# Optimization experiments

Hardware: AMD Instinct MI355X
Metric: run time of the kernel (lower is better)

## Reference

```python
import jax, jax.numpy as jnp
import numpy as np

NUM_HEADS = 8


def _conv1x1(x, W, b):
    # 1x1 conv == per-pixel linear: x [N,C,H,W], W [O,C], b [O]
    return jnp.einsum('nchw,oc->nohw', x, W) + b[None, :, None, None]


def setup_inputs() -> dict:
    key = jax.random.key(0)
    ks = jax.random.split(key, 10)
    C = 512
    s = 1.0 / np.sqrt(C)  # keep pre-softmax logits in a sane range
    return {
        'x': jax.random.normal(ks[0], (2, C, 64, 64), dtype=jnp.float32),
        'Wq': jax.random.normal(ks[1], (C, C), dtype=jnp.float32) * s,
        'bq': jax.random.normal(ks[2], (C,), dtype=jnp.float32) * 0.01,
        'Wk': jax.random.normal(ks[3], (C, C), dtype=jnp.float32) * s,
        'bk': jax.random.normal(ks[4], (C,), dtype=jnp.float32) * 0.01,
        'Wv': jax.random.normal(ks[5], (C, C), dtype=jnp.float32) * s,
        'bv': jax.random.normal(ks[6], (C,), dtype=jnp.float32) * 0.01,
        'Wo': jax.random.normal(ks[7], (C, C), dtype=jnp.float32) * s,
        'bo': jax.random.normal(ks[8], (C,), dtype=jnp.float32) * 0.01,
        'gamma': jax.random.normal(ks[9], (1,), dtype=jnp.float32),
    }


def reference(x, Wq, bq, Wk, bk, Wv, bv, Wo, bo, gamma):
    N, C, H, W = x.shape
    nh = NUM_HEADS
    hd = C // nh
    S = H * W
    scale = 1.0 / (hd ** 0.5)
    # Projections via 1x1 conv, then split heads over flattened spatial tokens
    Q = _conv1x1(x, Wq, bq).reshape(N, nh, hd, S).transpose(0, 1, 3, 2)  # [N,h,S,d]
    K = _conv1x1(x, Wk, bk).reshape(N, nh, hd, S)                         # [N,h,d,S]
    V = _conv1x1(x, Wv, bv).reshape(N, nh, hd, S).transpose(0, 1, 3, 2)  # [N,h,S,d]
    attn = jax.nn.softmax(jnp.einsum('nhsd,nhdt->nhst', Q, K) * scale, axis=-1)
    out = jnp.einsum('nhst,nhtd->nhsd', attn, V)                          # [N,h,S,d]
    out = out.transpose(0, 1, 3, 2).reshape(N, C, H, W)
    out = _conv1x1(out, Wo, bo)
    return gamma[0] * out + x
```

## Files before the change

kernel.cpp:

```cpp
#include <hip/hip_runtime.h>
#include <hip/hip_bf16.h>

typedef __attribute__((ext_vector_type(4))) float f32x4;
typedef __attribute__((ext_vector_type(16))) float f32x16;
typedef __attribute__((ext_vector_type(8))) short s16x8;
typedef __attribute__((ext_vector_type(4))) unsigned short us16x4;
typedef __attribute__((ext_vector_type(4))) unsigned int u32x4;

#define C_DIM 512
#define S_DIM 4096
#define NB 2
#define NH 8
#define HD 64

#define QSCALE 0.1803368801111244f

__device__ __forceinline__ unsigned short f2bf(float f) {
    union { float f; unsigned u; } v; v.f = f;
    unsigned r = v.u + 0x7FFFu + ((v.u >> 16) & 1u);
    return (unsigned short)(r >> 16);
}

__device__ __forceinline__ float bf2f(unsigned short u) {
    union { unsigned u; float f; } v; v.u = ((unsigned)u) << 16;
    return v.f;
}

__device__ __forceinline__ float dev_exp2(float x) {
    float r;
    asm("v_exp_f32 %0, %1" : "=v"(r) : "v"(x));
    return r;
}

__device__ __forceinline__ unsigned cvt_pk_bf16(float lo, float hi) {
    unsigned r;
    asm("v_cvt_pk_bf16_f32 %0, %1, %2" : "=v"(r) : "v"(lo), "v"(hi));
    return r;
}

__device__ __forceinline__ void lane_swap(unsigned& a, unsigned& b) {
    asm("v_permlane32_swap_b32 %0, %1" : "+v"(a), "+v"(b));
}

__device__ __forceinline__ void gload_lds16(const void* g, void* l) {
    __builtin_amdgcn_global_load_lds(
        (const __attribute__((address_space(1))) void*)g,
        (__attribute__((address_space(3))) void*)l, 16, 0, 0);
}

__global__ __launch_bounds__(256) void wconv_kernel(
    const float* __restrict__ Wq, const float* __restrict__ Wk,
    const float* __restrict__ Wv, const float* __restrict__ Wo,
    unsigned short* __restrict__ Wb) {
    int i = blockIdx.x * 256 + threadIdx.x;
    int y = blockIdx.y;
    const float* src = (y == 0) ? Wq : (y == 1) ? Wk : (y == 2) ? Wv : Wo;
    Wb[(size_t)y * 262144 + i] = f2bf(src[i]);
}

__global__ __launch_bounds__(256) void xpose_kernel(
    const float* __restrict__ x, unsigned short* __restrict__ Xt) {
    __shared__ float tile[32][33];
    int n = blockIdx.z;
    int s0 = blockIdx.x * 32;
    int c0 = blockIdx.y * 32;
    int tx = threadIdx.x & 31;
    int ty = threadIdx.x >> 5;
#pragma unroll
    for (int r = 0; r < 4; ++r) {
        int c = c0 + ty + r * 8;
        tile[ty + r * 8][tx] = x[((size_t)n * C_DIM + c) * S_DIM + s0 + tx];
    }
    __syncthreads();
#pragma unroll
    for (int r = 0; r < 4; ++r) {
        int s = s0 + ty + r * 8;
        Xt[((size_t)n * S_DIM + s) * C_DIM + c0 + tx] = f2bf(tile[tx][ty + r * 8]);
    }
}

__global__ __launch_bounds__(256) void qkv_gemm_kernel(
    const unsigned short* __restrict__ Wb, const unsigned short* __restrict__ Xt,
    const float* __restrict__ bq, const float* __restrict__ bk, const float* __restrict__ bv,
    unsigned short* __restrict__ Qt, unsigned short* __restrict__ Kt,
    unsigned short* __restrict__ Vb) {
    __shared__ unsigned short As[128 * 64];
    __shared__ unsigned short Bs[128 * 64];
    int w = blockIdx.z >> 1;
    int n = blockIdx.z & 1;
    const unsigned short* A = Wb + (size_t)w * 262144;
    const unsigned short* B = Xt + (size_t)n * S_DIM * C_DIM;
    int tid = threadIdx.x;
    int wid = tid >> 6, lane = tid & 63;
    int wm = wid >> 1, wn = wid & 1;
    int lr = lane & 15, lq = lane >> 4;
    int bm = blockIdx.y * 128, bt = blockIdx.x * 128;
    int r_in = lane >> 3, c8 = (lane & 7) * 8;

    f32x4 zero = {0.f, 0.f, 0.f, 0.f};
    f32x4 acc[4][4];
#pragma unroll
    for (int i = 0; i < 4; ++i)
#pragma unroll
        for (int j = 0; j < 4; ++j) acc[i][j] = zero;

    for (int ks = 0; ks < 8; ++ks) {
#pragma unroll
        for (int q = 0; q < 4; ++q) {
            int row = wid * 32 + q * 8;
            gload_lds16(A + (size_t)(bm + row + r_in) * C_DIM + ks * 64 + c8, &As[row * 64]);
            gload_lds16(B + (size_t)(bt + row + r_in) * C_DIM + ks * 64 + c8, &Bs[row * 64]);
        }
        __syncthreads();
#pragma unroll
        for (int kk = 0; kk < 2; ++kk) {
            s16x8 af[4], bf[4];
#pragma unroll
            for (int i = 0; i < 4; ++i)
                af[i] = *(const s16x8*)&As[(wm * 64 + i * 16 + lr) * 64 + kk * 32 + lq * 8];
#pragma unroll
            for (int j = 0; j < 4; ++j)
                bf[j] = *(const s16x8*)&Bs[(wn * 64 + j * 16 + lr) * 64 + kk * 32 + lq * 8];
#pragma unroll
            for (int i = 0; i < 4; ++i)
#pragma unroll
                for (int j = 0; j < 4; ++j)
                    acc[i][j] = __builtin_amdgcn_mfma_f32_16x16x32_bf16(af[i], bf[j], acc[i][j], 0, 0, 0);
        }
        __syncthreads();
    }

    const float* bias = (w == 0) ? bq : (w == 1) ? bk : bv;
#pragma unroll
    for (int i = 0; i < 4; ++i) {
        int obase = bm + wm * 64 + i * 16 + lq * 4;
#pragma unroll
        for (int j = 0; j < 4; ++j) {
            int t = bt + wn * 64 + j * 16 + lr;
            if (w == 0) {
                us16x4 pk;
#pragma unroll
                for (int r = 0; r < 4; ++r)
                    pk[r] = f2bf((acc[i][j][r] + bias[obase + r]) * QSCALE);
                int h = obase >> 6, d = obase & 63;
                *(us16x4*)&Qt[(((size_t)(n * NH + h) * S_DIM) + t) * HD + d] = pk;
            } else if (w == 1) {
                us16x4 pk;
#pragma unroll
                for (int r = 0; r < 4; ++r) pk[r] = f2bf(acc[i][j][r] + bias[obase + r]);
                int h = obase >> 6, d = obase & 63;
                *(us16x4*)&Kt[(((size_t)(n * NH + h) * S_DIM) + t) * HD + d] = pk;
            } else {
#pragma unroll
                for (int r = 0; r < 4; ++r) {
                    int o = obase + r;
                    Vb[((size_t)(n * C_DIM + o)) * S_DIM + t] = f2bf(acc[i][j][r] + bias[o]);
                }
            }
        }
    }
}

__global__ __launch_bounds__(256) void attn_kernel(
    const unsigned short* __restrict__ Qt, const unsigned short* __restrict__ Kt,
    const unsigned short* __restrict__ Vb, unsigned short* __restrict__ Opart,
    float* __restrict__ Lpart) {
    __shared__ unsigned short Ks[2][64 * 64];
    __shared__ unsigned short Vs[2][64 * 64];
    int tid = threadIdx.x, wid = tid >> 6, lane = tid & 63;
    int l31 = lane & 31, hi = lane >> 5;
    int radj = (l31 & 7) ^ ((l31 >> 3) & 3);

    int bidl = blockIdx.x;
    int swz = (bidl & 7) * 128 + (bidl >> 3);
    int nh = swz >> 6;
    int rem = swz & 63;
    int qb = rem >> 1;
    int half = rem & 1;
    int n = nh >> 3, h = nh & 7;
    int qrow0 = qb * 128 + wid * 32;
    int kvbase = half * 2048;

    const unsigned short* Qh = Qt + (size_t)nh * S_DIM * HD;
    const unsigned short* Kh = Kt + (size_t)nh * S_DIM * HD;
    const unsigned short* Vh = Vb + ((size_t)(n * C_DIM + h * HD)) * S_DIM;

    s16x8 qf[4];
#pragma unroll
    for (int st = 0; st < 4; ++st)
        qf[st] = *(const s16x8*)&Qh[((size_t)(qrow0 + l31)) * HD + st * 16 + hi * 8];

    s16x8 ones;
#pragma unroll
    for (int r = 0; r < 8; ++r) ones[r] = (short)0x3F80;

    f32x16 Oacc[2], Lacc;
#pragma unroll
    for (int jm = 0; jm < 2; ++jm)
#pragma unroll
        for (int r = 0; r < 16; ++r) Oacc[jm][r] = 0.f;
#pragma unroll
    for (int r = 0; r < 16; ++r) Lacc[r] = 0.f;

    int srow0 = tid >> 3, sslot = tid & 7;
    int wslot = (sslot ^ (srow0 & 7) ^ ((srow0 >> 3) & 3)) * 8;

    s16x8 kreg[2], vreg[2];
#pragma unroll
    for (int q = 0; q < 2; ++q) {
        int row = srow0 + q * 32;
        kreg[q] = *(const s16x8*)&Kh[((size_t)(kvbase + row)) * HD + sslot * 8];
        vreg[q] = *(const s16x8*)&Vh[((size_t)row) * S_DIM + kvbase + sslot * 8];
    }
#pragma unroll
    for (int q = 0; q < 2; ++q) {
        int row = srow0 + q * 32;
        *(s16x8*)&Ks[0][row * 64 + wslot] = kreg[q];
        *(s16x8*)&Vs[0][row * 64 + wslot] = vreg[q];
    }
    __syncthreads();

    for (int kt = 0; kt < 32; ++kt) {
        int cur = kt & 1;
        if (kt < 31) {
#pragma unroll
            for (int q = 0; q < 2; ++q) {
                int row = srow0 + q * 32;
                kreg[q] = *(const s16x8*)&Kh[((size_t)(kvbase + (kt + 1) * 64 + row)) * HD + sslot * 8];
                vreg[q] = *(const s16x8*)&Vh[((size_t)row) * S_DIM + kvbase + (kt + 1) * 64 + sslot * 8];
            }
        }

        f32x16 s_[2];
#pragma unroll
        for (int jm = 0; jm < 2; ++jm) {
#pragma unroll
            for (int r = 0; r < 16; ++r) s_[jm][r] = 0.f;
            int arow = jm * 32 + l31;
#pragma unroll
            for (int st = 0; st < 4; ++st) {
                s16x8 kf = *(const s16x8*)&Ks[cur][arow * 64 + ((2 * st + hi) ^ radj) * 8];
                s_[jm] = __builtin_amdgcn_mfma_f32_32x32x16_bf16(kf, qf[st], s_[jm], 0, 0, 0);
            }
        }

        s16x8 pf[2][2];
#pragma unroll
        for (int jm = 0; jm < 2; ++jm) {
            unsigned pk0 = cvt_pk_bf16(dev_exp2(s_[jm][0]),  dev_exp2(s_[jm][1]));
            unsigned pk1 = cvt_pk_bf16(dev_exp2(s_[jm][2]),  dev_exp2(s_[jm][3]));
            unsigned pk2 = cvt_pk_bf16(dev_exp2(s_[jm][4]),  dev_exp2(s_[jm][5]));
            unsigned pk3 = cvt_pk_bf16(dev_exp2(s_[jm][6]),  dev_exp2(s_[jm][7]));
            unsigned pk4 = cvt_pk_bf16(dev_exp2(s_[jm][8]),  dev_exp2(s_[jm][9]));
            unsigned pk5 = cvt_pk_bf16(dev_exp2(s_[jm][10]), dev_exp2(s_[jm][11]));
            unsigned pk6 = cvt_pk_bf16(dev_exp2(s_[jm][12]), dev_exp2(s_[jm][13]));
            unsigned pk7 = cvt_pk_bf16(dev_exp2(s_[jm][14]), dev_exp2(s_[jm][15]));
            lane_swap(pk2, pk0);
            lane_swap(pk3, pk1);
            lane_swap(pk6, pk4);
            lane_swap(pk7, pk5);
            u32x4 w0 = {pk0, pk1, pk2, pk3};
            u32x4 w1 = {pk4, pk5, pk6, pk7};
            pf[jm][0] = __builtin_bit_cast(s16x8, w0);
            pf[jm][1] = __builtin_bit_cast(s16x8, w1);
        }

#pragma unroll
        for (int jm = 0; jm < 2; ++jm)
#pragma unroll
            for (int st = 0; st < 2; ++st)
                Lacc = __builtin_amdgcn_mfma_f32_32x32x16_bf16(ones, pf[jm][st], Lacc, 0, 0, 0);

#pragma unroll
        for (int jm2 = 0; jm2 < 2; ++jm2) {
            int vrow = jm2 * 32 + l31;
#pragma unroll
            for (int jm = 0; jm < 2; ++jm)
#pragma unroll
                for (int st = 0; st < 2; ++st) {
                    s16x8 vf = *(const s16x8*)&Vs[cur][vrow * 64 + ((jm * 4 + st * 2 + hi) ^ radj) * 8];
                    Oacc[jm2] = __builtin_amdgcn_mfma_f32_32x32x16_bf16(vf, pf[jm][st], Oacc[jm2], 0, 0, 0);
                }
        }

        if (kt < 31) {
            int nxt = cur ^ 1;
#pragma unroll
            for (int q = 0; q < 2; ++q) {
                int row = srow0 + q * 32;
                *(s16x8*)&Ks[nxt][row * 64 + wslot] = kreg[q];
                *(s16x8*)&Vs[nxt][row * 64 + wslot] = vreg[q];
            }
            __syncthreads();
        }
    }

    int token = qrow0 + l31;
    unsigned short* obase = Opart + (((size_t)(half * 16 + nh) * S_DIM + token) * HD);
#pragma unroll
    for (int jm2 = 0; jm2 < 2; ++jm2)
#pragma unroll
        for (int rq = 0; rq < 4; ++rq) {
            int d = jm2 * 32 + 8 * rq + 4 * hi;
            us16x4 pk;
#pragma unroll
            for (int r = 0; r < 4; ++r) pk[r] = f2bf(Oacc[jm2][rq * 4 + r]);
            *(us16x4*)&obase[d] = pk;
        }
    if (hi == 0)
        Lpart[(size_t)(half * 16 + nh) * S_DIM + token] = Lacc[0];
}

__global__ __launch_bounds__(256) void combine_kernel(
    const unsigned short* __restrict__ Opart, const float* __restrict__ Lpart,
    unsigned short* __restrict__ Ot) {
    int g = blockIdx.x * 256 + threadIdx.x;
    int d4 = (g & 15) * 4;
    int s = (g >> 4) & 4095;
    int nh = g >> 16;
    size_t base0 = ((size_t)nh * S_DIM + s) * HD + d4;
    size_t base1 = base0 + (size_t)16 * S_DIM * HD;
    us16x4 o0 = *(const us16x4*)&Opart[base0];
    us16x4 o1 = *(const us16x4*)&Opart[base1];
    float l = Lpart[(size_t)nh * S_DIM + s] + Lpart[(size_t)(16 + nh) * S_DIM + s];
    float inv = 1.f / l;
    int n = nh >> 3, h = nh & 7;
    us16x4 pk;
#pragma unroll
    for (int r = 0; r < 4; ++r) pk[r] = f2bf((bf2f(o0[r]) + bf2f(o1[r])) * inv);
    *(us16x4*)&Ot[((size_t)n * S_DIM + s) * C_DIM + h * HD + d4] = pk;
}

__global__ __launch_bounds__(256) void out_gemm_kernel(
    const unsigned short* __restrict__ Wb, const unsigned short* __restrict__ Ot,
    const float* __restrict__ bo, const float* __restrict__ gamma,
    const float* __restrict__ xin, float* __restrict__ out) {
    __shared__ unsigned short As[128 * 64];
    __shared__ unsigned short Bs[128 * 64];
    int n = blockIdx.z;
    const unsigned short* A = Wb + (size_t)3 * 262144;
    const unsigned short* B = Ot + (size_t)n * S_DIM * C_DIM;
    int tid = threadIdx.x;
    int wid = tid >> 6, lane = tid & 63;
    int wm = wid >> 1, wn = wid & 1;
    int lr = lane & 15, lq = lane >> 4;
    int bm = blockIdx.y * 128, bt = blockIdx.x * 128;
    int r_in = lane >> 3, c8 = (lane & 7) * 8;

    f32x4 zero = {0.f, 0.f, 0.f, 0.f};
    f32x4 acc[4][4];
#pragma unroll
    for (int i = 0; i < 4; ++i)
#pragma unroll
        for (int j = 0; j < 4; ++j) acc[i][j] = zero;

    for (int ks = 0; ks < 8; ++ks) {
#pragma unroll
        for (int q = 0; q < 4; ++q) {
            int row = wid * 32 + q * 8;
            gload_lds16(A + (size_t)(bm + row + r_in) * C_DIM + ks * 64 + c8, &As[row * 64]);
            gload_lds16(B + (size_t)(bt + row + r_in) * C_DIM + ks * 64 + c8, &Bs[row * 64]);
        }
        __syncthreads();
#pragma unroll
        for (int kk = 0; kk < 2; ++kk) {
            s16x8 af[4], bf[4];
#pragma unroll
            for (int i = 0; i < 4; ++i)
                af[i] = *(const s16x8*)&As[(wm * 64 + i * 16 + lr) * 64 + kk * 32 + lq * 8];
#pragma unroll
            for (int j = 0; j < 4; ++j)
                bf[j] = *(const s16x8*)&Bs[(wn * 64 + j * 16 + lr) * 64 + kk * 32 + lq * 8];
#pragma unroll
            for (int i = 0; i < 4; ++i)
#pragma unroll
                for (int j = 0; j < 4; ++j)
                    acc[i][j] = __builtin_amdgcn_mfma_f32_16x16x32_bf16(af[i], bf[j], acc[i][j], 0, 0, 0);
        }
        __syncthreads();
    }

    float g = gamma[0];
#pragma unroll
    for (int i = 0; i < 4; ++i) {
        int obase = bm + wm * 64 + i * 16 + lq * 4;
#pragma unroll
        for (int j = 0; j < 4; ++j) {
            int t = bt + wn * 64 + j * 16 + lr;
#pragma unroll
            for (int r = 0; r < 4; ++r) {
                int o = obase + r;
                size_t idx = ((size_t)(n * C_DIM + o)) * S_DIM + t;
                out[idx] = g * (acc[i][j][r] + bo[o]) + xin[idx];
            }
        }
    }
}

extern "C" void kernel_launch(void* const* d_in, const int* in_sizes, int n_in,
                              void* d_out, int out_size, void* d_ws, size_t ws_size,
                              hipStream_t stream) {
    const float* x  = (const float*)d_in[0];
    const float* Wq = (const float*)d_in[1];
    const float* bq = (const float*)d_in[2];
    const float* Wk = (const float*)d_in[3];
    const float* bk = (const float*)d_in[4];
    const float* Wv = (const float*)d_in[5];
    const float* bv = (const float*)d_in[6];
    const float* Wo = (const float*)d_in[7];
    const float* bo = (const float*)d_in[8];
    const float* gamma = (const float*)d_in[9];
    float* out = (float*)d_out;

    char* ws = (char*)d_ws;
    unsigned short* Wb = (unsigned short*)ws;
    unsigned short* Xt = (unsigned short*)(ws + ((size_t)2  << 20));
    unsigned short* Qt = (unsigned short*)(ws + ((size_t)10 << 20));
    unsigned short* Kt = (unsigned short*)(ws + ((size_t)18 << 20));
    unsigned short* Vb = (unsigned short*)(ws + ((size_t)26 << 20));
    unsigned short* Ot = (unsigned short*)(ws + ((size_t)34 << 20));
    unsigned short* Opart = (unsigned short*)(ws + ((size_t)42 << 20));
    float* Lpart = (float*)(ws + ((size_t)60 << 20));

    wconv_kernel<<<dim3(1024, 4), 256, 0, stream>>>(Wq, Wk, Wv, Wo, Wb);
    xpose_kernel<<<dim3(128, 16, 2), 256, 0, stream>>>(x, Xt);
    qkv_gemm_kernel<<<dim3(32, 4, 6), 256, 0, stream>>>(Wb, Xt, bq, bk, bv, Qt, Kt, Vb);
    attn_kernel<<<1024, 256, 0, stream>>>(Qt, Kt, Vb, Opart, Lpart);
    combine_kernel<<<4096, 256, 0, stream>>>(Opart, Lpart, Ot);
    out_gemm_kernel<<<dim3(32, 4, 2), 256, 0, stream>>>(Wb, Ot, bo, gamma, x, out);
}
```

Before: 157.5 us.

## Single-buffer K/V LDS tiles, raise MFMA wave priority, seed QK with zero accumulator

The attention kernel drops from double-buffered to single-buffered K/V tiles in shared memory, halving LDS use so more blocks can be resident per CU. Each iteration now stores the prefetched registers to LDS at the top, synchronises, and synchronises again at the end before the next overwrite. MFMA sections are wrapped in s_setprio so waves doing matrix math get issue priority over waves doing softmax or loads. The first QK MFMA takes a zero vector as accumulator instead of zeroing s_ in a separate loop. The cost is a second barrier per iteration and less overlap within a block, which is traded for occupancy.

```diff
diff --git a/kernel.cpp b/kernel.cpp
--- a/kernel.cpp
+++ b/kernel.cpp
@@ -165,8 +165,8 @@
     const unsigned short* __restrict__ Qt, const unsigned short* __restrict__ Kt,
     const unsigned short* __restrict__ Vb, unsigned short* __restrict__ Opart,
     float* __restrict__ Lpart) {
-    __shared__ unsigned short Ks[2][64 * 64];
-    __shared__ unsigned short Vs[2][64 * 64];
+    __shared__ unsigned short Ks[64 * 64];
+    __shared__ unsigned short Vs[64 * 64];
     int tid = threadIdx.x, wid = tid >> 6, lane = tid & 63;
     int l31 = lane & 31, hi = lane >> 5;
     int radj = (l31 & 7) ^ ((l31 >> 3) & 3);
@@ -193,6 +193,9 @@
     s16x8 ones;
 #pragma unroll
     for (int r = 0; r < 8; ++r) ones[r] = (short)0x3F80;
+    f32x16 fz;
+#pragma unroll
+    for (int r = 0; r < 16; ++r) fz[r] = 0.f;
 
     f32x16 Oacc[2], Lacc;
 #pragma unroll
@@ -212,16 +215,15 @@
         kreg[q] = *(const s16x8*)&Kh[((size_t)(kvbase + row)) * HD + sslot * 8];
         vreg[q] = *(const s16x8*)&Vh[((size_t)row) * S_DIM + kvbase + sslot * 8];
     }
-#pragma unroll
-    for (int q = 0; q < 2; ++q) {
-        int row = srow0 + q * 32;
-        *(s16x8*)&Ks[0][row * 64 + wslot] = kreg[q];
-        *(s16x8*)&Vs[0][row * 64 + wslot] = vreg[q];
-    }
-    __syncthreads();
 
     for (int kt = 0; kt < 32; ++kt) {
-        int cur = kt & 1;
+#pragma unroll
+        for (int q = 0; q < 2; ++q) {
+            int row = srow0 + q * 32;
+            *(s16x8*)&Ks[row * 64 + wslot] = kreg[q];
+            *(s16x8*)&Vs[row * 64 + wslot] = vreg[q];
+        }
+        __syncthreads();
         if (kt < 31) {
 #pragma unroll
             for (int q = 0; q < 2; ++q) {
@@ -232,17 +234,19 @@
         }
 
         f32x16 s_[2];
+        __builtin_amdgcn_s_setprio(1);
 #pragma unroll
         for (int jm = 0; jm < 2; ++jm) {
-#pragma unroll
-            for (int r = 0; r < 16; ++r) s_[jm][r] = 0.f;
             int arow = jm * 32 + l31;
-#pragma unroll
-            for (int st = 0; st < 4; ++st) {
-                s16x8 kf = *(const s16x8*)&Ks[cur][arow * 64 + ((2 * st + hi) ^ radj) * 8];
+            s16x8 kf0 = *(const s16x8*)&Ks[arow * 64 + ((hi) ^ radj) * 8];
+            s_[jm] = __builtin_amdgcn_mfma_f32_32x32x16_bf16(kf0, qf[0], fz, 0, 0, 0);
+#pragma unroll
+            for (int st = 1; st < 4; ++st) {
+                s16x8 kf = *(const s16x8*)&Ks[arow * 64 + ((2 * st + hi) ^ radj) * 8];
                 s_[jm] = __builtin_amdgcn_mfma_f32_32x32x16_bf16(kf, qf[st], s_[jm], 0, 0, 0);
             }
         }
+        __builtin_amdgcn_s_setprio(0);
 
         s16x8 pf[2][2];
 #pragma unroll
@@ -265,6 +269,7 @@
             pf[jm][1] = __builtin_bit_cast(s16x8, w1);
         }
 
+        __builtin_amdgcn_s_setprio(1);
 #pragma unroll
         for (int jm = 0; jm < 2; ++jm)
 #pragma unroll
@@ -278,21 +283,12 @@
             for (int jm = 0; jm < 2; ++jm)
 #pragma unroll
                 for (int st = 0; st < 2; ++st) {
-                    s16x8 vf = *(const s16x8*)&Vs[cur][vrow * 64 + ((jm * 4 + st * 2 + hi) ^ radj) * 8];
+                    s16x8 vf = *(const s16x8*)&Vs[vrow * 64 + ((jm * 4 + st * 2 + hi) ^ radj) * 8];
                     Oacc[jm2] = __builtin_amdgcn_mfma_f32_32x32x16_bf16(vf, pf[jm][st], Oacc[jm2], 0, 0, 0);
                 }
         }
-
-        if (kt < 31) {
-            int nxt = cur ^ 1;
-#pragma unroll
-            for (int q = 0; q < 2; ++q) {
-                int row = srow0 + q * 32;
-                *(s16x8*)&Ks[nxt][row * 64 + wslot] = kreg[q];
-                *(s16x8*)&Vs[nxt][row * 64 + wslot] = vreg[q];
-            }
-            __syncthreads();
-        }
+        __builtin_amdgcn_s_setprio(0);
+        __syncthreads();
     }
 
     int token = qrow0 + l31;
```

Result: slower. 166.4 us (+5.7%).
